# Kernel optimization log

Measured on AMD Instinct MI355X. Metric: run time of the kernel, lower is better.

The kernel has to match this reference:

```python
import math
import jax, jax.numpy as jnp
import numpy as np

# Matryoshka nested sizes (num_heads == 1, kv_groups == 1)
QK_SIZES = [512, 1024, 1536, 2048]
HEAD_SIZES = [512, 1024, 1536, 2048]
D_IN = 2048   # input_sizes[-1]
D_OUT = 2048  # output_sizes[-1]
NEG = -1e9


def setup_inputs() -> dict:
    key = jax.random.key(0)
    ks = jax.random.split(key, 5)
    B, S = 4, 2048
    x = jax.random.normal(ks[0], (B, S, D_IN), dtype=jnp.float32)
    mask = jnp.tril(jnp.ones((S, S), dtype=bool))  # causal boolean mask
    scale = 0.02
    Wq = jax.random.normal(ks[1], (D_IN, QK_SIZES[-1]), dtype=jnp.float32) * scale
    Wk = jax.random.normal(ks[2], (D_IN, QK_SIZES[-1]), dtype=jnp.float32) * scale
    Wv = jax.random.normal(ks[3], (D_IN, HEAD_SIZES[-1]), dtype=jnp.float32) * scale
    Wo = jax.random.normal(ks[4], (HEAD_SIZES[-1], D_OUT), dtype=jnp.float32) * scale
    return {"x": x, "mask": mask, "Wq": Wq, "Wk": Wk, "Wv": Wv, "Wo": Wo}


def reference(x, mask, Wq, Wk, Wv, Wo):
    # x: [B, S, D_IN]; num_heads == 1 so we keep heads implicit.
    q = x @ Wq  # [B, S, qk_last]
    k = x @ Wk  # [B, S, qk_last]
    v = x @ Wv  # [B, S, head_last]
    mask_add = jnp.where(mask, 0.0, NEG).astype(x.dtype)  # [S, S]

    outs = []
    cum = None  # cumulative QK^T across nested qk slices
    prev_qk = 0
    prev_h = 0
    for qk, h in zip(QK_SIZES, HEAD_SIZES):
        dp = jnp.einsum("bqd,bkd->bqk", q[..., prev_qk:qk], k[..., prev_qk:qk])
        cum = dp if cum is None else cum + dp  # [B, S, S]
        logits = cum * (1.0 / math.sqrt(qk)) + mask_add
        attn = jax.nn.softmax(logits, axis=-1)
        outs.append(jnp.einsum("bqk,bkd->bqd", attn, v[..., prev_h:h]))
        prev_qk, prev_h = qk, h
    o = jnp.concatenate(outs, axis=-1)  # [B, S, head_last]
    return o @ Wo  # [B, S, D_OUT]
```

## Files before the change

kernel.cpp:

```cpp
#include <hip/hip_runtime.h>


typedef __attribute__((ext_vector_type(8))) short bf16x8;
typedef __attribute__((ext_vector_type(4))) float f32x4;
typedef unsigned short u16;
typedef unsigned int u32;

__device__ __forceinline__ u16 f2bf(float f) {
  union { float f; u32 u; } v; v.f = f;
  u32 r = v.u + 0x7fffu + ((v.u >> 16) & 1u);
  return (u16)(r >> 16);
}
__device__ __forceinline__ float bf2f(u16 b) {
  union { u32 u; float f; } v; v.u = ((u32)b) << 16;
  return v.f;
}
struct alignas(16) U16x8 { u16 v[8]; };
struct alignas(8) U16x4 { u16 v[4]; };

#define GLDS(gp, lp)                                                      \
  __builtin_amdgcn_global_load_lds(                                       \
      (const __attribute__((address_space(1))) void*)(gp),                \
      (__attribute__((address_space(3))) void*)(lp), 16, 0, 0)


__global__ __launch_bounds__(256) void conv_f32_bf16(const float* __restrict__ in,
                                                     u16* __restrict__ out) {
  size_t i = ((size_t)blockIdx.x * 256 + threadIdx.x) * 8;
  float4 a = *(const float4*)(in + i);
  float4 b = *(const float4*)(in + i + 4);
  U16x8 w;
  w.v[0] = f2bf(a.x); w.v[1] = f2bf(a.y); w.v[2] = f2bf(a.z); w.v[3] = f2bf(a.w);
  w.v[4] = f2bf(b.x); w.v[5] = f2bf(b.y); w.v[6] = f2bf(b.z); w.v[7] = f2bf(b.w);
  *(U16x8*)(out + i) = w;
}

__global__ __launch_bounds__(256) void transpose_conv4(const float* __restrict__ W0,
                                                       const float* __restrict__ W1,
                                                       const float* __restrict__ W2,
                                                       const float* __restrict__ W3,
                                                       u16* __restrict__ out) {
  const int D = 2048;
  const float* in = (blockIdx.z == 0) ? W0 : (blockIdx.z == 1) ? W1
                  : (blockIdx.z == 2) ? W2 : W3;
  u16* o = out + (size_t)blockIdx.z * D * D;
  __shared__ float t[32][33];
  int bx = blockIdx.x * 32, by = blockIdx.y * 32;
  int tx = threadIdx.x & 31, ty = threadIdx.x >> 5;
#pragma unroll
  for (int i = 0; i < 32; i += 8)
    t[ty + i][tx] = in[(size_t)(by + ty + i) * D + bx + tx];
  __syncthreads();
#pragma unroll
  for (int i = 0; i < 32; i += 8)
    o[(size_t)(bx + ty + i) * D + by + tx] = f2bf(t[tx][ty + i]);
}

template <bool OUT_BF16>
__global__ __launch_bounds__(512, 2) void gemm8p(
    const u16* __restrict__ A, int lda,
    const u16* __restrict__ B, int ldb,
    void* __restrict__ Cv, int ldc,
    int nmat, long long sBm, long long sCm, int vt) {
  extern __shared__ char smem[];
  u16* const S = (u16*)smem;

  const u32 wg = blockIdx.x;
  const int n0 = (int)(wg & 7u) * 256;
  const u32 c = wg >> 3;
  const int mat = (int)(c % (u32)nmat);
  const int m0 = (int)(c / (u32)nmat) * 256;
  B += (size_t)mat * sBm;

  const int tid = threadIdx.x;
  const int lane = tid & 63, wave = tid >> 6;
  const int wm = (wave >> 2) * 128;
  const int wn = (wave & 3) * 64;
  const int fr = lane & 15, kgrp = lane >> 4;
  const u32 lo = (u32)(wave * 1024);

  const int srow = tid >> 2;
  const int g = (tid & 3) ^ ((srow >> 1) & 3);
  const u16* gA = A + (size_t)(m0 + srow) * lda + g * 8;
  const u16* gB = B + (size_t)(n0 + srow) * ldb + g * 8;

  const int rbase = (kgrp ^ ((fr >> 1) & 3)) * 8;
  const int aoff = (wm + fr) * 32 + rbase;
  const int boff = 32768 + (wn + fr) * 32 + rbase;

#define STG8(ISB, slot, koff) do {                                       \
    char* d_ = (char*)smem + ((ISB) ? 65536 : 0) + (slot) * 16384 + lo;  \
    const u16* gp_ = (ISB) ? gB : gA;                                    \
    const int ld_ = (ISB) ? ldb : lda;                                   \
    GLDS(gp_ + (koff), d_);                                              \
    GLDS(gp_ + (size_t)128 * ld_ + (koff), d_ + 8192);                   \
  } while (0)

#define PH8(LP, kb, DOSTG, WC) do {                                      \
    constexpr int sl_ = (LP) >> 1;                                       \
    constexpr int mh_ = (LP) & 1;                                        \
    if (mh_ == 0) {                                                      \
      _Pragma("unroll") for (int n_ = 0; n_ < 4; ++n_)                   \
        fB[n_] = *(const bf16x8*)&S[boff + sl_ * 8192 + n_ * 512];       \
    }                                                                    \
    _Pragma("unroll") for (int a_ = 0; a_ < 4; ++a_)                     \
      fA[a_] = *(const bf16x8*)&S[aoff + sl_ * 8192 + mh_ * 2048 + a_ * 512]; \
    if (DOSTG) STG8(mh_, (3 + sl_) & 3, (kb) + (3 + sl_) * 32);          \
    if ((WC) == 4) asm volatile("s_waitcnt vmcnt(4)" ::: "memory");      \
    else if ((WC) == 0) asm volatile("s_waitcnt vmcnt(0)" ::: "memory"); \
    __builtin_amdgcn_s_barrier();                                        \
    asm volatile("s_waitcnt lgkmcnt(0)" ::: "memory");                   \
    __builtin_amdgcn_sched_barrier(0);                                   \
    __builtin_amdgcn_s_setprio(1);                                       \
    _Pragma("unroll") for (int a_ = 0; a_ < 4; ++a_)                     \
      _Pragma("unroll") for (int n_ = 0; n_ < 4; ++n_)                   \
        acc[mh_ * 4 + a_][n_] = __builtin_amdgcn_mfma_f32_16x16x32_bf16( \
            fA[a_], fB[n_], acc[mh_ * 4 + a_][n_], 0, 0, 0);             \
    __builtin_amdgcn_s_setprio(0);                                       \
    __builtin_amdgcn_s_barrier();                                        \
    __builtin_amdgcn_sched_barrier(0);                                   \
  } while (0)

  f32x4 acc[8][4];
#pragma unroll
  for (int m = 0; m < 8; ++m)
#pragma unroll
    for (int n = 0; n < 4; ++n)
#pragma unroll
      for (int j = 0; j < 4; ++j) acc[m][n][j] = 0.f;

  bf16x8 fA[4], fB[4];

  STG8(0, 0, 0);   STG8(1, 0, 0);
  STG8(0, 1, 32);  STG8(1, 1, 32);
  STG8(0, 2, 64);  STG8(1, 2, 64);
  asm volatile("s_waitcnt vmcnt(8)" ::: "memory");
  __builtin_amdgcn_s_barrier();
  __builtin_amdgcn_sched_barrier(0);

  for (int i = 0; i < 15; ++i) {
    const int kb = i * 128;
    PH8(0, kb, 1, -1);  PH8(1, kb, 1, 4);
    PH8(2, kb, 1, -1);  PH8(3, kb, 1, 4);
    PH8(4, kb, 1, -1);  PH8(5, kb, 1, 4);
    PH8(6, kb, 1, -1);  PH8(7, kb, 1, 4);
  }
  {
    const int kb = 15 * 128;
    PH8(0, kb, 1, -1);  PH8(1, kb, 1, 4);
    PH8(2, kb, 0, -1);  PH8(3, kb, 0, -1);
    PH8(4, kb, 0, -1);  PH8(5, kb, 0, 0);
    PH8(6, kb, 0, -1);  PH8(7, kb, 0, -1);
  }
#undef PH8
#undef STG8

  const int cl = lane & 15, rb = (lane >> 4) * 4;
  if (OUT_BF16) {
    if (vt && mat == 2) {
      __builtin_amdgcn_s_barrier();
      u16* VT = (u16*)Cv + 3 * sCm;
      u16* W = S + wave * 2176;
#pragma unroll
      for (int n = 0; n < 4; ++n) {
#pragma unroll
        for (int m = 0; m < 8; ++m) {
          U16x4 pk;
#pragma unroll
          for (int j = 0; j < 4; ++j) pk.v[j] = f2bf(acc[m][n][j]);
          *(U16x4*)&W[cl * 136 + m * 16 + rb] = pk;
        }
        asm volatile("s_waitcnt lgkmcnt(0)" ::: "memory");
        __builtin_amdgcn_sched_barrier(0);
#pragma unroll
        for (int step = 0; step < 4; ++step) {
          const int cc = step * 4 + (lane >> 4);
          U16x8 v = *(const U16x8*)&W[cc * 136 + (lane & 15) * 8];
          const int gcol = n0 + wn + n * 16 + cc;
          const int r0 = m0 + wm + (lane & 15) * 8;
          const int b = r0 >> 11, rr = r0 & 2047;
          *(U16x8*)&VT[(size_t)b * 4194304ull + (size_t)gcol * 2048 + rr] = v;
        }
        asm volatile("s_waitcnt lgkmcnt(0)" ::: "memory");
        __builtin_amdgcn_sched_barrier(0);
      }
    } else {
      u16* C = (u16*)Cv + (size_t)mat * sCm;
#pragma unroll
      for (int m = 0; m < 8; ++m)
#pragma unroll
        for (int n = 0; n < 4; ++n)
#pragma unroll
          for (int j = 0; j < 4; ++j)
            C[(size_t)(m0 + wm + m * 16 + rb + j) * ldc + (n0 + wn + n * 16 + cl)] =
                f2bf(acc[m][n][j]);
    }
  } else {
    float* C = (float*)Cv + (size_t)mat * sCm;
#pragma unroll
    for (int m = 0; m < 8; ++m)
#pragma unroll
      for (int n = 0; n < 4; ++n)
#pragma unroll
        for (int j = 0; j < 4; ++j)
          C[(size_t)(m0 + wm + m * 16 + rb + j) * ldc + (n0 + wn + n * 16 + cl)] =
              acc[m][n][j];
  }
}

__global__ __launch_bounds__(256) void qk_mega(
    const u16* __restrict__ A, const u16* __restrict__ B,
    u16* __restrict__ snapA, u16* __restrict__ snapB,
    float scaleA, float scaleB,
    const u16* __restrict__ initSrc, float initScale) {
  const int lda = 2048;
  const int m0 = blockIdx.y * 128, n0 = blockIdx.x * 128;
  if (n0 >= m0 + 128) return;
  const size_t zWE = (size_t)blockIdx.z * 4194304ull;
  extern __shared__ char smem[];
  u16* const As = (u16*)smem;
  u16* const Bs = (u16*)(smem + 32768);

  const int tid = threadIdx.x;
  const int lane = tid & 63, wave = tid >> 6;
  const int wm = (wave >> 1) * 64, wn = (wave & 1) * 64;
  const int fr = lane & 15;
  const int col = lane & 15, rb = (lane >> 4) * 4;
  const u32 lo = (u32)(wave * 1024);

  const int srow = tid >> 2;
  const int ssl = (tid & 3) ^ ((srow >> 1) & 3);
  const u16* gA0 = A + zWE + (size_t)(m0 + srow) * lda + ssl * 8;
  const u16* gA1 = gA0 + (size_t)64 * lda;
  const u16* gB0 = B + zWE + (size_t)(n0 + srow) * lda + ssl * 8;
  const u16* gB1 = gB0 + (size_t)64 * lda;

  const int koe = ((lane >> 4) ^ ((fr >> 1) & 3)) * 8;

#define QSTG(slot, kOff) do {                                             \
    char* la = (char*)As + (slot) * 8192 + lo;                            \
    char* lb = (char*)Bs + (slot) * 8192 + lo;                            \
    GLDS(gA0 + (kOff), la);                                               \
    GLDS(gA1 + (kOff), la + 4096);                                        \
    GLDS(gB0 + (kOff), lb);                                               \
    GLDS(gB1 + (kOff), lb + 4096);                                        \
  } while (0)

#define QREADF(FA, FB, sl) do {                                           \
    const u16* as_ = As + (sl) * 4096;                                    \
    const u16* bs_ = Bs + (sl) * 4096;                                    \
    _Pragma("unroll") for (int n_ = 0; n_ < 4; ++n_)                      \
      FB[n_] = *(const bf16x8*)&bs_[((wn + n_ * 16 + fr) << 5) + koe];    \
    _Pragma("unroll") for (int m_ = 0; m_ < 4; ++m_)                      \
      FA[m_] = *(const bf16x8*)&as_[((wm + m_ * 16 + fr) << 5) + koe];    \
  } while (0)

#define QMMCL(FA, FB) do {                                                \
    __builtin_amdgcn_s_setprio(1);                                        \
    _Pragma("unroll") for (int m_ = 0; m_ < 4; ++m_)                      \
    _Pragma("unroll") for (int n_ = 0; n_ < 4; ++n_)                      \
      acc[m_][n_] = __builtin_amdgcn_mfma_f32_16x16x32_bf16(              \
          FA[m_], FB[n_], acc[m_][n_], 0, 0, 0);                          \
    __builtin_amdgcn_s_setprio(0);                                        \
  } while (0)

#define QITER(tt, CA, CB, NA, NB) do {                                    \
    if ((tt) + 3 < 32)                                                    \
      asm volatile("s_waitcnt lgkmcnt(8)" ::: "memory");                  \
    if ((tt) <= 29)                                                       \
      asm volatile("s_waitcnt vmcnt(4)" ::: "memory");                    \
    else if ((tt) == 30)                                                  \
      asm volatile("s_waitcnt vmcnt(0)" ::: "memory");                    \
    if ((tt) <= 30) {                                                     \
      __builtin_amdgcn_s_barrier();                                       \
      __builtin_amdgcn_sched_barrier(0);                                  \
    }                                                                     \
    if ((tt) + 3 < 32) QSTG(((tt) + 3) & 3, ((tt) + 3) * 32);             \
    if ((tt) + 1 < 32) QREADF(NA, NB, ((tt) + 1) & 3);                    \
    QMMCL(CA, CB);                                                        \
  } while (0)

  f32x4 acc[4][4];
  if (initSrc) {
    const u16* ip = initSrc + zWE;
#pragma unroll
    for (int m = 0; m < 4; ++m)
#pragma unroll
      for (int n = 0; n < 4; ++n)
#pragma unroll
        for (int j = 0; j < 4; ++j)
          acc[m][n][j] = bf2f(ip[(size_t)(m0 + wm + m * 16 + rb + j) * 2048 +
                                 (n0 + wn + n * 16 + col)]) * initScale;
  } else {
#pragma unroll
    for (int m = 0; m < 4; ++m)
#pragma unroll
      for (int n = 0; n < 4; ++n)
#pragma unroll
        for (int j = 0; j < 4; ++j) acc[m][n][j] = 0.f;
  }

#define SNAPW(ptr, scl)                                                                \
  do {                                                                                 \
    u16* sp = (ptr) + zWE;                                                             \
    _Pragma("unroll") for (int m = 0; m < 4; ++m)                                      \
    _Pragma("unroll") for (int n = 0; n < 4; ++n)                                      \
    _Pragma("unroll") for (int j = 0; j < 4; ++j)                                      \
        sp[(size_t)(m0 + wm + m * 16 + rb + j) * 2048 + (n0 + wn + n * 16 + col)] =    \
            f2bf(acc[m][n][j] * (scl));                                                \
  } while (0)

  bf16x8 fA0[4], fB0[4], fA1[4], fB1[4];
  QSTG(0, 0);
  QSTG(1, 32);
  QSTG(2, 64);
  asm volatile("s_waitcnt vmcnt(8)" ::: "memory");
  __builtin_amdgcn_s_barrier();
  __builtin_amdgcn_sched_barrier(0);
  QREADF(fA0, fB0, 0);

  for (int tt = 0; tt < 32; tt += 2) {
    QITER(tt, fA0, fB0, fA1, fB1);
    QITER(tt + 1, fA1, fB1, fA0, fB0);
    if (tt == 14) SNAPW(snapA, scaleA);
  }
  SNAPW(snapB, scaleB);
#undef QITER
#undef QMMCL
#undef QREADF
#undef QSTG
#undef SNAPW
}

__global__ __launch_bounds__(256) void gemm_pv(
    const u16* __restrict__ A0, const u16* __restrict__ A1,
    const u16* __restrict__ vT, u16* __restrict__ o, int s0) {
  const int z = blockIdx.z;
  const int half = z >> 2, b = z & 3, s = s0 + half;
  const u16* A = (half ? A1 : A0) + (size_t)b * 4194304ull;
  const u16* B = vT + (size_t)b * 4194304ull + (size_t)s * 512 * 2048;
  u16* C = o + (size_t)b * 4194304ull + s * 512;

  const int n0 = blockIdx.x * 128, m0 = (15 - blockIdx.y) * 128;
  const int NT = (m0 + 128) >> 5;
  extern __shared__ char smem[];
  u16* const As = (u16*)smem;
  u16* const Bs = (u16*)(smem + 32768);

  const int tid = threadIdx.x;
  const int lane = tid & 63, wave = tid >> 6;
  const int wm = (wave >> 1) * 64, wn = (wave & 1) * 64;
  const int fr = lane & 15;
  const u32 lo = (u32)(wave * 1024);

  const int srow = tid >> 2;
  const int ssl = (tid & 3) ^ ((srow >> 1) & 3);
  const u16* gA0 = A + (size_t)(m0 + srow) * 2048 + ssl * 8;
  const u16* gA1 = gA0 + (size_t)64 * 2048;
  const u16* gB0 = B + (size_t)(n0 + srow) * 2048 + ssl * 8;
  const u16* gB1 = gB0 + (size_t)64 * 2048;

  const int koe = ((lane >> 4) ^ ((fr >> 1) & 3)) * 8;

#define PSTG(slot, kOff) do {                                             \
    char* la = (char*)As + (slot) * 8192 + lo;                            \
    char* lb = (char*)Bs + (slot) * 8192 + lo;                            \
    GLDS(gA0 + (kOff), la);                                               \
    GLDS(gA1 + (kOff), la + 4096);                                        \
    GLDS(gB0 + (kOff), lb);                                               \
    GLDS(gB1 + (kOff), lb + 4096);                                        \
  } while (0)

#define PREADF(FA, FB, sl) do {                                           \
    const u16* as_ = As + (sl) * 4096;                                    \
    const u16* bs_ = Bs + (sl) * 4096;                                    \
    _Pragma("unroll") for (int n_ = 0; n_ < 4; ++n_)                      \
      FB[n_] = *(const bf16x8*)&bs_[((wn + n_ * 16 + fr) << 5) + koe];    \
    _Pragma("unroll") for (int m_ = 0; m_ < 4; ++m_)                      \
      FA[m_] = *(const bf16x8*)&as_[((wm + m_ * 16 + fr) << 5) + koe];    \
  } while (0)

#define PMMCL(FA, FB) do {                                                \
    __builtin_amdgcn_s_setprio(1);                                        \
    _Pragma("unroll") for (int m_ = 0; m_ < 4; ++m_)                      \
    _Pragma("unroll") for (int n_ = 0; n_ < 4; ++n_)                      \
      acc[m_][n_] = __builtin_amdgcn_mfma_f32_16x16x32_bf16(              \
          FA[m_], FB[n_], acc[m_][n_], 0, 0, 0);                          \
    __builtin_amdgcn_s_setprio(0);                                        \
  } while (0)

#define PITER(tt, CA, CB, NA, NB) do {                                    \
    if ((tt) + 3 < NT)                                                    \
      asm volatile("s_waitcnt lgkmcnt(8)" ::: "memory");                  \
    if ((tt) <= NT - 3)                                                   \
      asm volatile("s_waitcnt vmcnt(4)" ::: "memory");                    \
    else if ((tt) == NT - 2)                                              \
      asm volatile("s_waitcnt vmcnt(0)" ::: "memory");                    \
    if ((tt) <= NT - 2) {                                                 \
      __builtin_amdgcn_s_barrier();                                       \
      __builtin_amdgcn_sched_barrier(0);                                  \
    }                                                                     \
    if ((tt) + 3 < NT) PSTG(((tt) + 3) & 3, ((tt) + 3) * 32);             \
    if ((tt) + 1 < NT) PREADF(NA, NB, ((tt) + 1) & 3);                    \
    PMMCL(CA, CB);                                                        \
  } while (0)

  f32x4 acc[4][4];
#pragma unroll
  for (int m = 0; m < 4; ++m)
#pragma unroll
    for (int n = 0; n < 4; ++n)
#pragma unroll
      for (int j = 0; j < 4; ++j) acc[m][n][j] = 0.f;

  bf16x8 fA0[4], fB0[4], fA1[4], fB1[4];
  PSTG(0, 0);
  PSTG(1, 32);
  PSTG(2, 64);
  asm volatile("s_waitcnt vmcnt(8)" ::: "memory");
  __builtin_amdgcn_s_barrier();
  __builtin_amdgcn_sched_barrier(0);
  PREADF(fA0, fB0, 0);

  for (int tt = 0; tt < NT; tt += 2) {
    PITER(tt, fA0, fB0, fA1, fB1);
    PITER(tt + 1, fA1, fB1, fA0, fB0);
  }
#undef PITER
#undef PMMCL
#undef PREADF
#undef PSTG

  const int col = lane & 15, rb = (lane >> 4) * 4;
#pragma unroll
  for (int m = 0; m < 4; ++m)
#pragma unroll
    for (int n = 0; n < 4; ++n)
#pragma unroll
      for (int j = 0; j < 4; ++j)
        C[(size_t)(m0 + wm + m * 16 + rb + j) * 2048 + (n0 + wn + n * 16 + col)] =
            f2bf(acc[m][n][j]);
}

__global__ __launch_bounds__(256) void softmax_dual(const u16* __restrict__ in0,
                                                    u16* __restrict__ out0,
                                                    const u16* __restrict__ in1,
                                                    u16* __restrict__ out1) {
  const int S = 2048;
  const int y = blockIdx.y;
  const u16* in  = (y < 4) ? in0  : in1;
  u16* out       = (y < 4) ? out0 : out1;
  const size_t WEz = (size_t)S * S * (y & 3);
  const int r = blockIdx.x;
  const int tid = threadIdx.x;
  const int lane = tid & 63, wave = tid >> 6;
  const int c0 = tid * 8;
  const int nvalid = r + 1;
  const int nwrite = (r & ~127) + 128;
  const u16* rowp = in + WEz + (size_t)r * S;

  float x[8];
  if (c0 < nvalid) {
    U16x8 a = *(const U16x8*)(rowp + c0);
#pragma unroll
    for (int i = 0; i < 8; ++i) x[i] = bf2f(a.v[i]);
  } else {
#pragma unroll
    for (int i = 0; i < 8; ++i) x[i] = 0.f;
  }

  float mx = -3e38f;
#pragma unroll
  for (int i = 0; i < 8; ++i)
    if (c0 + i < nvalid) mx = fmaxf(mx, x[i]);
#pragma unroll
  for (int off = 32; off > 0; off >>= 1) mx = fmaxf(mx, __shfl_xor(mx, off));
  __shared__ float redm[4], reds[4];
  if (lane == 0) redm[wave] = mx;
  __syncthreads();
  mx = fmaxf(fmaxf(redm[0], redm[1]), fmaxf(redm[2], redm[3]));

  float e[8], sum = 0.f;
#pragma unroll
  for (int i = 0; i < 8; ++i) {
    e[i] = (c0 + i < nvalid) ? __expf(x[i] - mx) : 0.f;
    sum += e[i];
  }
#pragma unroll
  for (int off = 32; off > 0; off >>= 1) sum += __shfl_xor(sum, off);
  if (lane == 0) reds[wave] = sum;
  __syncthreads();
  sum = reds[0] + reds[1] + reds[2] + reds[3];
  float inv = 1.f / sum;

  if (c0 < nwrite) {
    U16x8 w;
#pragma unroll
    for (int i = 0; i < 8; ++i) w.v[i] = f2bf(e[i] * inv);
    *(U16x8*)(out + WEz + (size_t)r * S + c0) = w;
  }
}

extern "C" void kernel_launch(void* const* d_in, const int* in_sizes, int n_in,
                              void* d_out, int out_size, void* d_ws, size_t ws_size,
                              hipStream_t stream) {
  (void)in_sizes; (void)n_in; (void)out_size; (void)ws_size;
  const float* x  = (const float*)d_in[0];
  const float* Wq = (const float*)d_in[2];
  const float* Wk = (const float*)d_in[3];
  const float* Wv = (const float*)d_in[4];
  const float* Wo = (const float*)d_in[5];
  float* out = (float*)d_out;

  char* w = (char*)d_ws;
  const size_t R  = 33554432ull;
  const long long WE = 4194304LL;

  u16* xb  = (u16*)(w);
  u16* wT  = (u16*)(w + R);
  u16* wqT = wT;
  u16* woT = wT + 3 * WE;
  u16* q   = (u16*)(w + 2 * R);
  u16* kk  = (u16*)(w + 3 * R);
  u16* o   = (u16*)(w + 4 * R);
  u16* vT  = (u16*)(w + 5 * R);
  u16* attnx = xb;
  u16* slot0 = (u16*)d_out;
  u16* slot1 = slot0 + 16777216ull;

  const float sc0 = 1.0f / sqrtf(512.0f);
  const float sc1 = 1.0f / sqrtf(1024.0f);
  const float sc2 = 1.0f / sqrtf(1536.0f);
  const float sc3 = 1.0f / sqrtf(2048.0f);

  hipFuncSetAttribute(reinterpret_cast<const void*>(&gemm8p<true>),
                      hipFuncAttributeMaxDynamicSharedMemorySize, 131072);
  hipFuncSetAttribute(reinterpret_cast<const void*>(&gemm8p<false>),
                      hipFuncAttributeMaxDynamicSharedMemorySize, 131072);
  hipFuncSetAttribute(reinterpret_cast<const void*>(&qk_mega),
                      hipFuncAttributeMaxDynamicSharedMemorySize, 65536);
  hipFuncSetAttribute(reinterpret_cast<const void*>(&gemm_pv),
                      hipFuncAttributeMaxDynamicSharedMemorySize, 65536);

  conv_f32_bf16<<<8192, 256, 0, stream>>>(x, xb);
  transpose_conv4<<<dim3(64, 64, 4), 256, 0, stream>>>(Wq, Wk, Wv, Wo, wT);
  gemm8p<true><<<dim3(768), 512, 131072, stream>>>(
      xb, 2048, wqT, 2048, q, 2048, 3, WE, 16777216LL, 1);
  qk_mega<<<dim3(16, 16, 4), 256, 65536, stream>>>(q, kk, slot0, slot1, sc0, sc1,
                                                   nullptr, 0.f);
  softmax_dual<<<dim3(2048, 8), 256, 0, stream>>>(slot0, slot0, slot1, attnx);
  gemm_pv<<<dim3(4, 16, 8), 256, 65536, stream>>>(slot0, attnx, vT, o, 0);
  qk_mega<<<dim3(16, 16, 4), 256, 65536, stream>>>(q + 1024, kk + 1024, slot0,
                                                   slot1, sc2, sc3, slot1, 32.0f);
  softmax_dual<<<dim3(2048, 8), 256, 0, stream>>>(slot0, slot0, slot1, slot1);
  gemm_pv<<<dim3(4, 16, 8), 256, 65536, stream>>>(slot0, slot1, vT, o, 2);
  gemm8p<false><<<dim3(256), 512, 131072, stream>>>(
      o, 2048, woT, 2048, out, 2048, 1, 0LL, 0LL, 0);
}
```

Measured before the change: 498.4 us.

## Widen QK kernel tile to 128x256 with double-buffered LDS pipeline

Replaces the 128x128 QK^T tile kernel with a 128x256 variant in which each of the four waves covers all 128 rows and a 64-column strip. This raises data reuse per block and halves the number of blocks. The LDS pipeline drops from four stages to two, with a full vmcnt(0) wait and an extra barrier each iteration, and launch bounds now request two blocks per CU. The causal skip now works at 256-column granularity, so some tiles above the diagonal that were skipped before are now computed. Register pressure also rises from the larger accumulator.

Result: slower. 636.9 us (+27.8%).

```diff
diff --git a/kernel.cpp b/kernel.cpp
--- a/kernel.cpp
+++ b/kernel.cpp
@@ -208,92 +208,88 @@
   }
 }
 
-__global__ __launch_bounds__(256) void qk_mega(
+__global__ __launch_bounds__(256, 2) void qk256(
     const u16* __restrict__ A, const u16* __restrict__ B,
     u16* __restrict__ snapA, u16* __restrict__ snapB,
     float scaleA, float scaleB,
     const u16* __restrict__ initSrc, float initScale) {
-  const int lda = 2048;
-  const int m0 = blockIdx.y * 128, n0 = blockIdx.x * 128;
+  const int m0 = blockIdx.y * 128, n0 = blockIdx.x * 256;
   if (n0 >= m0 + 128) return;
   const size_t zWE = (size_t)blockIdx.z * 4194304ull;
   extern __shared__ char smem[];
   u16* const As = (u16*)smem;
-  u16* const Bs = (u16*)(smem + 32768);
+  u16* const Bs = (u16*)smem + 8192;
 
   const int tid = threadIdx.x;
   const int lane = tid & 63, wave = tid >> 6;
-  const int wm = (wave >> 1) * 64, wn = (wave & 1) * 64;
+  const int wn = (wave & 3) * 64;
   const int fr = lane & 15;
   const int col = lane & 15, rb = (lane >> 4) * 4;
   const u32 lo = (u32)(wave * 1024);
 
   const int srow = tid >> 2;
   const int ssl = (tid & 3) ^ ((srow >> 1) & 3);
-  const u16* gA0 = A + zWE + (size_t)(m0 + srow) * lda + ssl * 8;
-  const u16* gA1 = gA0 + (size_t)64 * lda;
-  const u16* gB0 = B + zWE + (size_t)(n0 + srow) * lda + ssl * 8;
-  const u16* gB1 = gB0 + (size_t)64 * lda;
+  const u16* gA = A + zWE + (size_t)(m0 + srow) * 2048 + ssl * 8;
+  const u16* gB = B + zWE + (size_t)(n0 + srow) * 2048 + ssl * 8;
 
   const int koe = ((lane >> 4) ^ ((fr >> 1) & 3)) * 8;
 
-#define QSTG(slot, kOff) do {                                             \
+#define KSTG(slot, kOff) do {                                             \
     char* la = (char*)As + (slot) * 8192 + lo;                            \
-    char* lb = (char*)Bs + (slot) * 8192 + lo;                            \
-    GLDS(gA0 + (kOff), la);                                               \
-    GLDS(gA1 + (kOff), la + 4096);                                        \
-    GLDS(gB0 + (kOff), lb);                                               \
-    GLDS(gB1 + (kOff), lb + 4096);                                        \
-  } while (0)
-
-#define QREADF(FA, FB, sl) do {                                           \
+    char* lb = (char*)Bs + (slot) * 16384 + lo;                           \
+    _Pragma("unroll") for (int j_ = 0; j_ < 2; ++j_)                      \
+      GLDS(gA + (size_t)j_ * 64 * 2048 + (kOff), la + j_ * 4096);         \
+    _Pragma("unroll") for (int j_ = 0; j_ < 4; ++j_)                      \
+      GLDS(gB + (size_t)j_ * 64 * 2048 + (kOff), lb + j_ * 4096);         \
+  } while (0)
+
+#define KREADF(FA, FB, sl) do {                                           \
     const u16* as_ = As + (sl) * 4096;                                    \
-    const u16* bs_ = Bs + (sl) * 4096;                                    \
+    const u16* bs_ = Bs + (sl) * 8192;                                    \
     _Pragma("unroll") for (int n_ = 0; n_ < 4; ++n_)                      \
       FB[n_] = *(const bf16x8*)&bs_[((wn + n_ * 16 + fr) << 5) + koe];    \
-    _Pragma("unroll") for (int m_ = 0; m_ < 4; ++m_)                      \
-      FA[m_] = *(const bf16x8*)&as_[((wm + m_ * 16 + fr) << 5) + koe];    \
-  } while (0)
-
-#define QMMCL(FA, FB) do {                                                \
+    _Pragma("unroll") for (int m_ = 0; m_ < 8; ++m_)                      \
+      FA[m_] = *(const bf16x8*)&as_[((m_ * 16 + fr) << 5) + koe];         \
+  } while (0)
+
+#define KMMCL(FA, FB) do {                                                \
     __builtin_amdgcn_s_setprio(1);                                        \
-    _Pragma("unroll") for (int m_ = 0; m_ < 4; ++m_)                      \
+    _Pragma("unroll") for (int m_ = 0; m_ < 8; ++m_)                      \
     _Pragma("unroll") for (int n_ = 0; n_ < 4; ++n_)                      \
       acc[m_][n_] = __builtin_amdgcn_mfma_f32_16x16x32_bf16(              \
           FA[m_], FB[n_], acc[m_][n_], 0, 0, 0);                          \
     __builtin_amdgcn_s_setprio(0);                                        \
   } while (0)
 
-#define QITER(tt, CA, CB, NA, NB) do {                                    \
-    if ((tt) + 3 < 32)                                                    \
-      asm volatile("s_waitcnt lgkmcnt(8)" ::: "memory");                  \
-    if ((tt) <= 29)                                                       \
-      asm volatile("s_waitcnt vmcnt(4)" ::: "memory");                    \
-    else if ((tt) == 30)                                                  \
-      asm volatile("s_waitcnt vmcnt(0)" ::: "memory");                    \
-    if ((tt) <= 30) {                                                     \
+#define KITER(tt, CA, CB, NA, NB) do {                                    \
+    if ((tt) + 1 < 32) KREADF(NA, NB, ((tt) + 1) & 1);                    \
+    if ((tt) + 2 < 32) {                                                  \
+      asm volatile("s_waitcnt lgkmcnt(12)" ::: "memory");                 \
       __builtin_amdgcn_s_barrier();                                       \
+      KSTG((tt) & 1, ((tt) + 2) * 32);                                    \
       __builtin_amdgcn_sched_barrier(0);                                  \
     }                                                                     \
-    if ((tt) + 3 < 32) QSTG(((tt) + 3) & 3, ((tt) + 3) * 32);             \
-    if ((tt) + 1 < 32) QREADF(NA, NB, ((tt) + 1) & 3);                    \
-    QMMCL(CA, CB);                                                        \
-  } while (0)
-
-  f32x4 acc[4][4];
+    KMMCL(CA, CB);                                                        \
+    if ((tt) + 2 < 32) {                                                  \
+      asm volatile("s_waitcnt vmcnt(0)" ::: "memory");                    \
+      __builtin_amdgcn_s_barrier();                                       \
+    }                                                                     \
+  } while (0)
+
+  f32x4 acc[8][4];
   if (initSrc) {
     const u16* ip = initSrc + zWE;
 #pragma unroll
-    for (int m = 0; m < 4; ++m)
+    for (int m = 0; m < 8; ++m)
 #pragma unroll
       for (int n = 0; n < 4; ++n)
 #pragma unroll
         for (int j = 0; j < 4; ++j)
-          acc[m][n][j] = bf2f(ip[(size_t)(m0 + wm + m * 16 + rb + j) * 2048 +
+          acc[m][n][j] = bf2f(ip[(size_t)(m0 + m * 16 + rb + j) * 2048 +
                                  (n0 + wn + n * 16 + col)]) * initScale;
   } else {
 #pragma unroll
-    for (int m = 0; m < 4; ++m)
+    for (int m = 0; m < 8; ++m)
 #pragma unroll
       for (int n = 0; n < 4; ++n)
 #pragma unroll
@@ -303,32 +299,31 @@
 #define SNAPW(ptr, scl)                                                                \
   do {                                                                                 \
     u16* sp = (ptr) + zWE;                                                             \
-    _Pragma("unroll") for (int m = 0; m < 4; ++m)                                      \
+    _Pragma("unroll") for (int m = 0; m < 8; ++m)                                      \
     _Pragma("unroll") for (int n = 0; n < 4; ++n)                                      \
     _Pragma("unroll") for (int j = 0; j < 4; ++j)                                      \
-        sp[(size_t)(m0 + wm + m * 16 + rb + j) * 2048 + (n0 + wn + n * 16 + col)] =    \
+        sp[(size_t)(m0 + m * 16 + rb + j) * 2048 + (n0 + wn + n * 16 + col)] =         \
             f2bf(acc[m][n][j] * (scl));                                                \
   } while (0)
 
-  bf16x8 fA0[4], fB0[4], fA1[4], fB1[4];
-  QSTG(0, 0);
-  QSTG(1, 32);
-  QSTG(2, 64);
-  asm volatile("s_waitcnt vmcnt(8)" ::: "memory");
+  bf16x8 fA0[8], fB0[4], fA1[8], fB1[4];
+  KSTG(0, 0);
+  KSTG(1, 32);
+  asm volatile("s_waitcnt vmcnt(0)" ::: "memory");
   __builtin_amdgcn_s_barrier();
   __builtin_amdgcn_sched_barrier(0);
-  QREADF(fA0, fB0, 0);
+  KREADF(fA0, fB0, 0);
 
   for (int tt = 0; tt < 32; tt += 2) {
-    QITER(tt, fA0, fB0, fA1, fB1);
-    QITER(tt + 1, fA1, fB1, fA0, fB0);
+    KITER(tt, fA0, fB0, fA1, fB1);
+    KITER(tt + 1, fA1, fB1, fA0, fB0);
     if (tt == 14) SNAPW(snapA, scaleA);
   }
   SNAPW(snapB, scaleB);
-#undef QITER
-#undef QMMCL
-#undef QREADF
-#undef QSTG
+#undef KITER
+#undef KMMCL
+#undef KREADF
+#undef KSTG
 #undef SNAPW
 }
 
@@ -537,8 +532,8 @@
                       hipFuncAttributeMaxDynamicSharedMemorySize, 131072);
   hipFuncSetAttribute(reinterpret_cast<const void*>(&gemm8p<false>),
                       hipFuncAttributeMaxDynamicSharedMemorySize, 131072);
-  hipFuncSetAttribute(reinterpret_cast<const void*>(&qk_mega),
-                      hipFuncAttributeMaxDynamicSharedMemorySize, 65536);
+  hipFuncSetAttribute(reinterpret_cast<const void*>(&qk256),
+                      hipFuncAttributeMaxDynamicSharedMemorySize, 49152);
   hipFuncSetAttribute(reinterpret_cast<const void*>(&gemm_pv),
                       hipFuncAttributeMaxDynamicSharedMemorySize, 65536);
 
@@ -546,12 +541,12 @@
   transpose_conv4<<<dim3(64, 64, 4), 256, 0, stream>>>(Wq, Wk, Wv, Wo, wT);
   gemm8p<true><<<dim3(768), 512, 131072, stream>>>(
       xb, 2048, wqT, 2048, q, 2048, 3, WE, 16777216LL, 1);
-  qk_mega<<<dim3(16, 16, 4), 256, 65536, stream>>>(q, kk, slot0, slot1, sc0, sc1,
-                                                   nullptr, 0.f);
+  qk256<<<dim3(8, 16, 4), 256, 49152, stream>>>(q, kk, slot0, slot1, sc0, sc1,
+                                                nullptr, 0.f);
   softmax_dual<<<dim3(2048, 8), 256, 0, stream>>>(slot0, slot0, slot1, attnx);
   gemm_pv<<<dim3(4, 16, 8), 256, 65536, stream>>>(slot0, attnx, vT, o, 0);
-  qk_mega<<<dim3(16, 16, 4), 256, 65536, stream>>>(q + 1024, kk + 1024, slot0,
-                                                   slot1, sc2, sc3, slot1, 32.0f);
+  qk256<<<dim3(8, 16, 4), 256, 49152, stream>>>(q + 1024, kk + 1024, slot0,
+                                                slot1, sc2, sc3, slot1, 32.0f);
   softmax_dual<<<dim3(2048, 8), 256, 0, stream>>>(slot0, slot0, slot1, slot1);
   gemm_pv<<<dim3(4, 16, 8), 256, 65536, stream>>>(slot0, slot1, vT, o, 2);
   gemm8p<false><<<dim3(256), 512, 131072, stream>>>(
```
